# Optimization experiments

Measured on AMD Instinct MI355X. Metric: run time of the kernel, lower is better.

## Reference

```python
import jax, jax.numpy as jnp
import numpy as np

BS, M, T, V = 16, 16, 32, 12000   # batch, max caps/video, max caption len, caption vocab
P, PV = 64, 20                    # program max len, program vocab


def setup_inputs() -> dict:
    key = jax.random.key(0)
    ks = jax.random.split(key, 10)
    gt_captions = jax.random.randint(ks[0], (BS, M, T), 0, V)
    gt_cap_lens = jax.random.randint(ks[1], (BS, M), 1, T + 1).astype(jnp.int32)
    pred_captions = jax.random.normal(ks[2], (BS, M, T, V), dtype=jnp.float32)
    gt_program = jax.random.randint(ks[3], (BS, P), 0, PV)
    gt_prog_len = jax.random.randint(ks[4], (BS,), 1, P + 1).astype(jnp.int32)
    pred_program = jax.random.normal(ks[5], (BS, P, PV), dtype=jnp.float32)
    gt_intervals = jnp.sort(jax.random.uniform(ks[6], (BS, M, 2), dtype=jnp.float32), axis=-1)
    pred_intervals = jnp.sort(jax.random.uniform(ks[7], (BS, M, 2), dtype=jnp.float32), axis=-1)
    gt_caps_count = jax.random.randint(ks[8], (BS,), 1, M + 1).astype(jnp.int32)
    pred_caps_count = jax.random.randint(ks[9], (BS,), 1, M + 1).astype(jnp.int32)
    return dict(gt_captions=gt_captions, gt_cap_lens=gt_cap_lens, pred_captions=pred_captions,
                gt_program=gt_program, gt_prog_len=gt_prog_len, pred_program=pred_program,
                gt_intervals=gt_intervals, pred_intervals=pred_intervals,
                gt_caps_count=gt_caps_count, pred_caps_count=pred_caps_count)


def reference(gt_captions, gt_cap_lens, pred_captions, gt_program, gt_prog_len,
              pred_program, gt_intervals, pred_intervals, gt_caps_count, pred_caps_count):
    # Instead of the torch python-loop ragged gather/concat, we compute the same
    # losses with validity masks (identical math: masked-out tokens contribute 0,
    # denominators are the exact ragged element counts).
    bs, m, t, v = pred_captions.shape
    # token valid iff position < cap_len AND caption index < caps_count
    tok_mask = (jnp.arange(t)[None, None, :] < gt_cap_lens[:, :, None]) & \
               (jnp.arange(m)[None, :, None] < gt_caps_count[:, None, None])
    logp = jax.nn.log_softmax(pred_captions, axis=-1)                       # [bs,m,t,V]
    tok_nll = -jnp.take_along_axis(logp, gt_captions[..., None], axis=-1)[..., 0]
    n_tok = jnp.maximum(tok_mask.sum(), 1).astype(tok_nll.dtype)
    cap_loss = jnp.sum(jnp.where(tok_mask, tok_nll, 0.0)) / n_tok           # CE mean

    # program CE over ragged prefixes
    p = pred_program.shape[1]
    pmask = jnp.arange(p)[None, :] < gt_prog_len[:, None]                   # [bs,P]
    plogp = jax.nn.log_softmax(pred_program, axis=-1)
    pnll = -jnp.take_along_axis(plogp, gt_program[..., None], axis=-1)[..., 0]
    prog_loss = jnp.sum(jnp.where(pmask, pnll, 0.0)) / jnp.maximum(pmask.sum(), 1).astype(pnll.dtype)

    # IoU loss over the first gt_caps_count[j] intervals of each sample
    cmask = jnp.arange(m)[None, :] < gt_caps_count[:, None]                 # [bs,m]
    inter = jnp.clip(jnp.minimum(pred_intervals[..., 1], gt_intervals[..., 1]) -
                     jnp.maximum(pred_intervals[..., 0], gt_intervals[..., 0]), 0.0)
    union = jnp.maximum(pred_intervals[..., 1], gt_intervals[..., 1]) - \
            jnp.minimum(pred_intervals[..., 0], gt_intervals[..., 0])
    iou = jnp.where(cmask, inter / jnp.maximum(union, 1e-8), 0.0)
    n_caps = jnp.maximum(gt_caps_count.sum(), 1).astype(iou.dtype)
    iou_loss = 1.0 - jnp.sum(iou) / n_caps                                  # IoU mean

    loss = cap_loss + prog_loss
    return (loss, cap_loss, prog_loss, iou_loss)
```

## Files before the change

### kernel.cpp

```cpp
#include <hip/hip_runtime.h>
#include <hip/hip_bf16.h>
#include <math.h>

#define BS 16
#define M  16
#define T  32
#define V  12000
#define P  64
#define PV 20

__global__ __launch_bounds__(256) void cap_loss_kernel(
    const float* __restrict__ pred,
    const int*   __restrict__ gt,
    const int*   __restrict__ cap_lens,
    const int*   __restrict__ caps_count,
    float*       __restrict__ acc)
{
    const int row = blockIdx.x;
    const int t   = row % T;
    const int bm  = row / T;
    const int m   = bm % M;
    const int b   = bm / M;

    if (t >= cap_lens[bm] || m >= caps_count[b]) return;

    const float4* p4 = (const float4*)(pred + (size_t)row * V);
    const int NV4 = V / 4;

    float lmax = -INFINITY;
    float lsum = 0.0f;
    for (int i = threadIdx.x; i < NV4; i += 256) {
        float4 x = p4[i];
        float m4 = fmaxf(fmaxf(x.x, x.y), fmaxf(x.z, x.w));
        float nm = fmaxf(lmax, m4);
        lsum = lsum * __expf(lmax - nm)
             + __expf(x.x - nm) + __expf(x.y - nm)
             + __expf(x.z - nm) + __expf(x.w - nm);
        lmax = nm;
    }

    for (int off = 32; off > 0; off >>= 1) {
        float om = __shfl_down(lmax, off, 64);
        float os = __shfl_down(lsum, off, 64);
        float nm = fmaxf(lmax, om);
        lsum = lsum * __expf(lmax - nm) + os * __expf(om - nm);
        lmax = nm;
    }

    __shared__ float sm[4], ss[4];
    const int wave = threadIdx.x >> 6;
    const int lane = threadIdx.x & 63;
    if (lane == 0) { sm[wave] = lmax; ss[wave] = lsum; }
    __syncthreads();

    if (threadIdx.x == 0) {
        float gm = sm[0], gs = ss[0];
        #pragma unroll
        for (int w = 1; w < 4; w++) {
            float nm = fmaxf(gm, sm[w]);
            gs = gs * __expf(gm - nm) + ss[w] * __expf(sm[w] - nm);
            gm = nm;
        }
        const float xg  = pred[(size_t)row * V + gt[row]];
        const float nll = logf(gs) + gm - xg;
        atomicAdd(acc, nll);
    }
}

__global__ __launch_bounds__(256) void prog_loss_kernel(
    const float* __restrict__ pred_prog,
    const int*   __restrict__ gt_prog,
    const int*   __restrict__ prog_len,
    float*       __restrict__ acc)
{
    const int idx = blockIdx.x * blockDim.x + threadIdx.x;
    const int p   = idx % P;
    const int b   = idx / P;

    float nll = 0.0f;
    if (p < prog_len[b]) {
        const float* row = pred_prog + (size_t)idx * PV;
        float mx = row[0];
        #pragma unroll
        for (int i = 1; i < PV; i++) mx = fmaxf(mx, row[i]);
        float s = 0.0f;
        #pragma unroll
        for (int i = 0; i < PV; i++) s += __expf(row[i] - mx);
        nll = logf(s) + mx - row[gt_prog[idx]];
    }
    for (int off = 32; off > 0; off >>= 1) nll += __shfl_down(nll, off, 64);
    if ((threadIdx.x & 63) == 0) atomicAdd(acc + 1, nll);
}

__global__ __launch_bounds__(256) void final_kernel(
    const int*   __restrict__ cap_lens,
    const int*   __restrict__ caps_count,
    const int*   __restrict__ prog_len,
    const float* __restrict__ gt_iv,
    const float* __restrict__ pred_iv,
    const float* __restrict__ acc,
    float*       __restrict__ out)
{
    const int idx = threadIdx.x;
    const int m = idx % M, b = idx / M;
    const int cc = caps_count[b];

    float ntok = (m < cc) ? (float)cap_lens[idx] : 0.0f;

    float iou = 0.0f;
    if (m < cc) {
        const float gs = gt_iv[idx * 2], ge = gt_iv[idx * 2 + 1];
        const float ps = pred_iv[idx * 2], pe = pred_iv[idx * 2 + 1];
        float inter = fminf(pe, ge) - fmaxf(ps, gs);
        inter = fmaxf(inter, 0.0f);
        const float uni = fmaxf(pe, ge) - fminf(ps, gs);
        iou = inter / fmaxf(uni, 1e-8f);
    }
    float nprog = (idx < BS) ? (float)prog_len[idx]   : 0.0f;
    float ncaps = (idx < BS) ? (float)caps_count[idx] : 0.0f;

    __shared__ float s_tok[256], s_iou[256], s_np[256], s_nc[256];
    s_tok[idx] = ntok; s_iou[idx] = iou; s_np[idx] = nprog; s_nc[idx] = ncaps;
    __syncthreads();
    for (int off = 128; off > 0; off >>= 1) {
        if (idx < off) {
            s_tok[idx] += s_tok[idx + off];
            s_iou[idx] += s_iou[idx + off];
            s_np[idx]  += s_np[idx + off];
            s_nc[idx]  += s_nc[idx + off];
        }
        __syncthreads();
    }
    if (idx == 0) {
        const float cap_loss  = acc[0] / fmaxf(s_tok[0], 1.0f);
        const float prog_loss = acc[1] / fmaxf(s_np[0], 1.0f);
        const float iou_loss  = 1.0f - s_iou[0] / fmaxf(s_nc[0], 1.0f);
        out[0] = cap_loss + prog_loss;
        out[1] = cap_loss;
        out[2] = prog_loss;
        out[3] = iou_loss;
    }
}

extern "C" void kernel_launch(void* const* d_in, const int* in_sizes, int n_in,
                              void* d_out, int out_size, void* d_ws, size_t ws_size,
                              hipStream_t stream) {
    const int*   gt_captions    = (const int*)  d_in[0];
    const int*   gt_cap_lens    = (const int*)  d_in[1];
    const float* pred_captions  = (const float*)d_in[2];
    const int*   gt_program     = (const int*)  d_in[3];
    const int*   gt_prog_len    = (const int*)  d_in[4];
    const float* pred_program   = (const float*)d_in[5];
    const float* gt_intervals   = (const float*)d_in[6];
    const float* pred_intervals = (const float*)d_in[7];
    const int*   gt_caps_count  = (const int*)  d_in[8];

    float* out = (float*)d_out;
    float* acc = (float*)d_ws;

    hipMemsetAsync(acc, 0, 2 * sizeof(float), stream);

    cap_loss_kernel<<<BS * M * T, 256, 0, stream>>>(
        pred_captions, gt_captions, gt_cap_lens, gt_caps_count, acc);

    prog_loss_kernel<<<(BS * P) / 256, 256, 0, stream>>>(
        pred_program, gt_program, gt_prog_len, acc);

    final_kernel<<<1, 256, 0, stream>>>(
        gt_cap_lens, gt_caps_count, gt_prog_len,
        gt_intervals, pred_intervals, acc, out);
}
```

Baseline: 486.6 us.

## Fuse caption and program loss kernels, replace atomics with per-row partials

Merges the caption-loss and program-loss kernels into one launch, with the program blocks appended after the caption rows. The memset is removed. Global float atomics are replaced by per-row partial sums written to workspace, and the final kernel reduces them with the same validity masks. The aim is to cut launch and memset overhead and atomic contention, at the cost of a larger serial reduction in the single-block final kernel.

```diff
diff --git a/kernel.cpp b/kernel.cpp
--- a/kernel.cpp
+++ b/kernel.cpp
@@ -9,87 +9,87 @@
 #define P  64
 #define PV 20
 
-__global__ __launch_bounds__(256) void cap_loss_kernel(
-    const float* __restrict__ pred,
-    const int*   __restrict__ gt,
+#define NCAP   (BS * M * T)
+#define NPROGB 4
+
+__global__ __launch_bounds__(256) void fused_loss_kernel(
+    const float* __restrict__ pred_cap,
+    const int*   __restrict__ gt_cap,
     const int*   __restrict__ cap_lens,
     const int*   __restrict__ caps_count,
-    float*       __restrict__ acc)
-{
-    const int row = blockIdx.x;
-    const int t   = row % T;
-    const int bm  = row / T;
-    const int m   = bm % M;
-    const int b   = bm / M;
-
-    if (t >= cap_lens[bm] || m >= caps_count[b]) return;
-
-    const float4* p4 = (const float4*)(pred + (size_t)row * V);
-    const int NV4 = V / 4;
-
-    float lmax = -INFINITY;
-    float lsum = 0.0f;
-    for (int i = threadIdx.x; i < NV4; i += 256) {
-        float4 x = p4[i];
-        float m4 = fmaxf(fmaxf(x.x, x.y), fmaxf(x.z, x.w));
-        float nm = fmaxf(lmax, m4);
-        lsum = lsum * __expf(lmax - nm)
-             + __expf(x.x - nm) + __expf(x.y - nm)
-             + __expf(x.z - nm) + __expf(x.w - nm);
-        lmax = nm;
-    }
-
-    for (int off = 32; off > 0; off >>= 1) {
-        float om = __shfl_down(lmax, off, 64);
-        float os = __shfl_down(lsum, off, 64);
-        float nm = fmaxf(lmax, om);
-        lsum = lsum * __expf(lmax - nm) + os * __expf(om - nm);
-        lmax = nm;
-    }
-
-    __shared__ float sm[4], ss[4];
-    const int wave = threadIdx.x >> 6;
-    const int lane = threadIdx.x & 63;
-    if (lane == 0) { sm[wave] = lmax; ss[wave] = lsum; }
-    __syncthreads();
-
-    if (threadIdx.x == 0) {
-        float gm = sm[0], gs = ss[0];
-        #pragma unroll
-        for (int w = 1; w < 4; w++) {
-            float nm = fmaxf(gm, sm[w]);
-            gs = gs * __expf(gm - nm) + ss[w] * __expf(sm[w] - nm);
-            gm = nm;
-        }
-        const float xg  = pred[(size_t)row * V + gt[row]];
-        const float nll = logf(gs) + gm - xg;
-        atomicAdd(acc, nll);
-    }
-}
-
-__global__ __launch_bounds__(256) void prog_loss_kernel(
     const float* __restrict__ pred_prog,
     const int*   __restrict__ gt_prog,
     const int*   __restrict__ prog_len,
-    float*       __restrict__ acc)
+    float*       __restrict__ ws)
 {
-    const int idx = blockIdx.x * blockDim.x + threadIdx.x;
-    const int p   = idx % P;
-    const int b   = idx / P;
+    const int bid = blockIdx.x;
+    __shared__ float sm[4], ss[4];
 
-    float nll = 0.0f;
-    if (p < prog_len[b]) {
-        const float* row = pred_prog + (size_t)idx * PV;
-        float mx = row[0];
-        #pragma unroll
-        for (int i = 1; i < PV; i++) mx = fmaxf(mx, row[i]);
-        float s = 0.0f;
-        #pragma unroll
-        for (int i = 0; i < PV; i++) s += __expf(row[i] - mx);
-        nll = logf(s) + mx - row[gt_prog[idx]];
+    if (bid < NCAP) {
+        const int t  = bid % T;
+        const int bm = bid / T;
+        const int m  = bm % M;
+        const int b  = bm / M;
+        if (t >= cap_lens[bm] || m >= caps_count[b]) return;
+
+        const float4* p4 = (const float4*)(pred_cap + (size_t)bid * V);
+        const int NV4 = V / 4;
+
+        float lmax = -INFINITY, lsum = 0.0f;
+        for (int i = threadIdx.x; i < NV4; i += 256) {
+            float4 x = p4[i];
+            float m4 = fmaxf(fmaxf(x.x, x.y), fmaxf(x.z, x.w));
+            float nm = fmaxf(lmax, m4);
+            lsum = lsum * __expf(lmax - nm)
+                 + __expf(x.x - nm) + __expf(x.y - nm)
+                 + __expf(x.z - nm) + __expf(x.w - nm);
+            lmax = nm;
+        }
+        for (int off = 32; off > 0; off >>= 1) {
+            float om = __shfl_down(lmax, off, 64);
+            float os = __shfl_down(lsum, off, 64);
+            float nm = fmaxf(lmax, om);
+            lsum = lsum * __expf(lmax - nm) + os * __expf(om - nm);
+            lmax = nm;
+        }
+        const int wave = threadIdx.x >> 6, lane = threadIdx.x & 63;
+        if (lane == 0) { sm[wave] = lmax; ss[wave] = lsum; }
+        __syncthreads();
+        if (threadIdx.x == 0) {
+            float gm = sm[0], gs = ss[0];
+            #pragma unroll
+            for (int w = 1; w < 4; w++) {
+                float nm = fmaxf(gm, sm[w]);
+                gs = gs * __expf(gm - nm) + ss[w] * __expf(sm[w] - nm);
+                gm = nm;
+            }
+            const float xg = pred_cap[(size_t)bid * V + gt_cap[bid]];
+            ws[bid] = logf(gs) + gm - xg;
+        }
+    } else {
+        const int pb  = bid - NCAP;
+        const int idx = pb * 256 + threadIdx.x;
+        const int p   = idx % P;
+        const int b   = idx / P;
+
+        float nll = 0.0f;
+        if (p < prog_len[b]) {
+            const float* row = pred_prog + (size_t)idx * PV;
+            float mx = row[0];
+            #pragma unroll
+            for (int i = 1; i < PV; i++) mx = fmaxf(mx, row[i]);
+            float s = 0.0f;
+            #pragma unroll
+            for (int i = 0; i < PV; i++) s += __expf(row[i] - mx);
+            nll = logf(s) + mx - row[gt_prog[idx]];
+        }
+        for (int off = 32; off > 0; off >>= 1) nll += __shfl_down(nll, off, 64);
+        const int wave = threadIdx.x >> 6, lane = threadIdx.x & 63;
+        if (lane == 0) ss[wave] = nll;
+        __syncthreads();
+        if (threadIdx.x == 0)
+            ws[NCAP + pb] = ss[0] + ss[1] + ss[2] + ss[3];
     }
-    for (int off = 32; off > 0; off >>= 1) nll += __shfl_down(nll, off, 64);
-    if ((threadIdx.x & 63) == 0) atomicAdd(acc + 1, nll);
 }
 
 __global__ __launch_bounds__(256) void final_kernel(
@@ -98,43 +98,58 @@
     const int*   __restrict__ prog_len,
     const float* __restrict__ gt_iv,
     const float* __restrict__ pred_iv,
-    const float* __restrict__ acc,
+    const float* __restrict__ ws,
     float*       __restrict__ out)
 {
-    const int idx = threadIdx.x;
-    const int m = idx % M, b = idx / M;
-    const int cc = caps_count[b];
+    const int tid = threadIdx.x;
+    __shared__ int   s_len[BS * M];
+    __shared__ int   s_cc[BS];
+    __shared__ float red[6][256];
 
-    float ntok = (m < cc) ? (float)cap_lens[idx] : 0.0f;
+    s_len[tid] = cap_lens[tid];
+    if (tid < BS) s_cc[tid] = caps_count[tid];
+    __syncthreads();
 
+    float cap_sum = 0.0f;
+    #pragma unroll
+    for (int k = 0; k < NCAP / 256; k++) {
+        const int r  = tid + k * 256;
+        const int t  = r % T;
+        const int bm = r / T;
+        const int m  = bm % M;
+        const int b  = bm / M;
+        if (t < s_len[bm] && m < s_cc[b]) cap_sum += ws[r];
+    }
+    float prog_sum = (tid < NPROGB) ? ws[NCAP + tid] : 0.0f;
+
+    const int m = tid % M, b = tid / M;
+    const bool cvalid = (m < s_cc[b]);
+    float ntok = cvalid ? (float)s_len[tid] : 0.0f;
     float iou = 0.0f;
-    if (m < cc) {
-        const float gs = gt_iv[idx * 2], ge = gt_iv[idx * 2 + 1];
-        const float ps = pred_iv[idx * 2], pe = pred_iv[idx * 2 + 1];
-        float inter = fminf(pe, ge) - fmaxf(ps, gs);
-        inter = fmaxf(inter, 0.0f);
+    if (cvalid) {
+        const float gs = gt_iv[tid * 2], ge = gt_iv[tid * 2 + 1];
+        const float ps = pred_iv[tid * 2], pe = pred_iv[tid * 2 + 1];
+        float inter = fmaxf(fminf(pe, ge) - fmaxf(ps, gs), 0.0f);
         const float uni = fmaxf(pe, ge) - fminf(ps, gs);
         iou = inter / fmaxf(uni, 1e-8f);
     }
-    float nprog = (idx < BS) ? (float)prog_len[idx]   : 0.0f;
-    float ncaps = (idx < BS) ? (float)caps_count[idx] : 0.0f;
+    float nprog = (tid < BS) ? (float)prog_len[tid] : 0.0f;
+    float ncaps = (tid < BS) ? (float)s_cc[tid]     : 0.0f;
 
-    __shared__ float s_tok[256], s_iou[256], s_np[256], s_nc[256];
-    s_tok[idx] = ntok; s_iou[idx] = iou; s_np[idx] = nprog; s_nc[idx] = ncaps;
+    red[0][tid] = cap_sum; red[1][tid] = prog_sum; red[2][tid] = ntok;
+    red[3][tid] = iou;     red[4][tid] = nprog;    red[5][tid] = ncaps;
     __syncthreads();
     for (int off = 128; off > 0; off >>= 1) {
-        if (idx < off) {
-            s_tok[idx] += s_tok[idx + off];
-            s_iou[idx] += s_iou[idx + off];
-            s_np[idx]  += s_np[idx + off];
-            s_nc[idx]  += s_nc[idx + off];
+        if (tid < off) {
+            #pragma unroll
+            for (int q = 0; q < 6; q++) red[q][tid] += red[q][tid + off];
         }
         __syncthreads();
     }
-    if (idx == 0) {
-        const float cap_loss  = acc[0] / fmaxf(s_tok[0], 1.0f);
-        const float prog_loss = acc[1] / fmaxf(s_np[0], 1.0f);
-        const float iou_loss  = 1.0f - s_iou[0] / fmaxf(s_nc[0], 1.0f);
+    if (tid == 0) {
+        const float cap_loss  = red[0][0] / fmaxf(red[2][0], 1.0f);
+        const float prog_loss = red[1][0] / fmaxf(red[4][0], 1.0f);
+        const float iou_loss  = 1.0f - red[3][0] / fmaxf(red[5][0], 1.0f);
         out[0] = cap_loss + prog_loss;
         out[1] = cap_loss;
         out[2] = prog_loss;
@@ -155,18 +170,14 @@
     const float* pred_intervals = (const float*)d_in[7];
     const int*   gt_caps_count  = (const int*)  d_in[8];
 
+    float* ws  = (float*)d_ws;
     float* out = (float*)d_out;
-    float* acc = (float*)d_ws;
 
-    hipMemsetAsync(acc, 0, 2 * sizeof(float), stream);
-
-    cap_loss_kernel<<<BS * M * T, 256, 0, stream>>>(
-        pred_captions, gt_captions, gt_cap_lens, gt_caps_count, acc);
-
-    prog_loss_kernel<<<(BS * P) / 256, 256, 0, stream>>>(
-        pred_program, gt_program, gt_prog_len, acc);
+    fused_loss_kernel<<<NCAP + NPROGB, 256, 0, stream>>>(
+        pred_captions, gt_captions, gt_cap_lens, gt_caps_count,
+        pred_program, gt_program, gt_prog_len, ws);
 
     final_kernel<<<1, 256, 0, stream>>>(
         gt_cap_lens, gt_caps_count, gt_prog_len,
-        gt_intervals, pred_intervals, acc, out);
+        gt_intervals, pred_intervals, ws, out);
 }
```

Measured after the change: 484.6 us. About the same (-0.4%).
